# Optimization experiments

Measured on AMD Instinct MI355X. Metric: run time of the kernel, lower is better.

The kernel has to match this reference:

```python
import jax, jax.numpy as jnp
import numpy as np

VOCAB = 32000
WORDVEC = 256
HIDDEN = 512
NULL_TOKEN = 0


def setup_inputs() -> dict:
    key = jax.random.key(0)
    ks = jax.random.split(key, 8)
    N, Tp1 = 16, 257
    captions = jax.random.randint(ks[0], (N, Tp1), 0, VOCAB, dtype=jnp.int64 if jax.config.jax_enable_x64 else jnp.int32)
    W_embed = jax.random.normal(ks[1], (VOCAB, WORDVEC), jnp.float32) / 100.0
    Wx = jax.random.normal(ks[2], (WORDVEC, 4 * HIDDEN), jnp.float32) / np.sqrt(WORDVEC).astype(np.float32)
    Wh = jax.random.normal(ks[3], (HIDDEN, 4 * HIDDEN), jnp.float32) / np.sqrt(HIDDEN).astype(np.float32)
    b = jnp.zeros((4 * HIDDEN,), jnp.float32)
    W_vocab = jax.random.normal(ks[4], (HIDDEN, VOCAB), jnp.float32) / np.sqrt(HIDDEN).astype(np.float32)
    b_vocab = jnp.zeros((VOCAB,), jnp.float32)
    h_init = jax.random.normal(ks[5], (HIDDEN,), jnp.float32)
    return {"captions": captions, "W_embed": W_embed, "Wx": Wx, "Wh": Wh,
            "b": b, "W_vocab": W_vocab, "b_vocab": b_vocab, "h_init": h_init}


def reference(captions, W_embed, Wx, Wh, b, W_vocab, b_vocab, h_init):
    cap_in = captions[:, :-1]   # [N, T]
    cap_out = captions[:, 1:]   # [N, T]
    mask = (cap_out != NULL_TOKEN).astype(jnp.float32)
    N = cap_in.shape[0]
    H = h_init.shape[0]

    # Embedding lookup: [N, T, D]
    x = W_embed[cap_in]
    # Precompute input projections as one big GEMM: [T, N, 4H]
    xw = jnp.einsum('ntd,dk->tnk', x, Wx) + b

    h0 = jnp.tile(h_init, (N, 1))          # [N, H]
    c0 = jnp.zeros_like(h0)                 # lstm_forward starts c at zeros

    def step(carry, a_x):
        h, c = carry
        a = a_x + h @ Wh                    # [N, 4H]
        i, f, o, g = jnp.split(a, 4, axis=-1)
        i = jax.nn.sigmoid(i)
        f = jax.nn.sigmoid(f)
        o = jax.nn.sigmoid(o)
        g = jnp.tanh(g)
        c = f * c + i * g
        h = o * jnp.tanh(c)
        return (h, c), h

    _, hs = jax.lax.scan(step, (h0, c0), xw)  # hs: [T, N, H]

    # Temporal affine: [N, T, V]
    logits = jnp.einsum('tnh,hv->ntv', hs, W_vocab) + b_vocab
    logp = jax.nn.log_softmax(logits, axis=-1)
    nll = -jnp.take_along_axis(logp, cap_out[..., None], axis=-1)[..., 0]
    loss = jnp.sum(nll * mask) / N
    return loss
```

## Files before the change

### kernel.cpp

```cpp
#include <hip/hip_runtime.h>

#define VOCAB   32000
#define WORDVEC 256
#define HIDDEN  512
#define TSTEPS  256
#define NBATCH  16
#define NROWS   (TSTEPS*NBATCH)
#define GATES   (4*HIDDEN)
#define NVB     125
#define NWG     32

typedef __attribute__((ext_vector_type(8))) short short8;
typedef __attribute__((ext_vector_type(4))) float f32x4;
typedef unsigned long long u64;

__device__ __forceinline__ unsigned short f2bf(float x){
    union { float f; unsigned int u; } v; v.f = x;
    unsigned int r = v.u + 0x7fffu + ((v.u >> 16) & 1u);
    return (unsigned short)(r >> 16);
}

__global__ __launch_bounds__(256) void wv_pack(const float* __restrict__ Wv, unsigned short* __restrict__ WvP){
    __shared__ float s[64][65];
    int v0 = blockIdx.x * 64;
    int k0 = blockIdx.y * 64;
    int tid = threadIdx.x;
    for (int i = 0; i < 16; ++i){
        int lin = tid + i*256;
        int kk = lin >> 6, vv = lin & 63;
        s[kk][vv] = Wv[(long)(k0+kk)*VOCAB + v0 + vv];
    }
    __syncthreads();
    for (int i = 0; i < 2; ++i){
        int lr = tid + i*256;
        int f  = lr >> 6;
        int vbl = f >> 1, ktl = f & 1;
        int L = lr & 63, q = L >> 4, ln = L & 15;
        short8 o;
        #pragma unroll
        for (int j = 0; j < 8; ++j)
            o[j] = (short)f2bf(s[ktl*32 + q*8 + j][vbl*16 + ln]);
        long vb = blockIdx.x*4 + vbl;
        long kt = blockIdx.y*2 + ktl;
        *(short8*)(WvP + ((vb*16 + kt)*64 + L)*8) = o;
    }
}

__global__ void whp_prep(const float* __restrict__ Wh, unsigned short* __restrict__ Whp){
    int w = blockIdx.x; int tid = threadIdx.x;
    for (int item = tid; item < 4096; item += 256){
        int f = item >> 6;
        int L = item & 63;
        int kt = f >> 2, nt = f & 3;
        int q = L >> 4, ln = L & 15;
        int col = nt*HIDDEN + w*16 + ln;
        short8 vvec;
        for (int jj = 0; jj < 8; ++jj){
            int k = kt*32 + q*8 + jj;
            vvec[jj] = (short)f2bf(Wh[(long)k*GATES + col]);
        }
        *(short8*)(Whp + ((long)w*4096 + item)*8) = vvec;
    }
}

__global__ void hg_init(const float* __restrict__ h_init, u64* __restrict__ hx){
    int p = blockIdx.x*256 + threadIdx.x;
    int fq = p >> 6;
    int j  = (p & 3) * 2;
    int u0 = (fq>>2)*32 + (fq&3)*8 + j;
    u64 pk = (u64)f2bf(h_init[u0]) | ((u64)f2bf(h_init[u0+1]) << 16);
    hx[p] = pk;
}

__global__ __launch_bounds__(256) void embed_xw(const int* __restrict__ captions,
        const float* __restrict__ Wemb, const float* __restrict__ Wx,
        const float* __restrict__ b, float* __restrict__ xw){
    __shared__ float xs[8][WORDVEC];
    __shared__ int toks[8];
    int tid = threadIdx.x;
    int r0 = blockIdx.x * 8;
    if (tid < 8){
        int r = r0 + tid; int t = r >> 4, n = r & 15;
        toks[tid] = captions[n*257 + t];
    }
    __syncthreads();
    for (int i = 0; i < 8; ++i){
        int lin = tid + i*256;
        int ri = lin >> 8, d = lin & 255;
        xs[ri][d] = Wemb[(long)toks[ri]*WORDVEC + d];
    }
    __syncthreads();
    float4 b0 = *(const float4*)(b + tid*4);
    float4 b1 = *(const float4*)(b + 1024 + tid*4);
    float acc[8][8];
    for (int ri = 0; ri < 8; ++ri){
        acc[ri][0]=b0.x; acc[ri][1]=b0.y; acc[ri][2]=b0.z; acc[ri][3]=b0.w;
        acc[ri][4]=b1.x; acc[ri][5]=b1.y; acc[ri][6]=b1.z; acc[ri][7]=b1.w;
    }
    for (int d = 0; d < WORDVEC; ++d){
        float4 w0 = *(const float4*)(Wx + (long)d*GATES + tid*4);
        float4 w1 = *(const float4*)(Wx + (long)d*GATES + 1024 + tid*4);
        #pragma unroll
        for (int ri = 0; ri < 8; ++ri){
            float xv = xs[ri][d];
            acc[ri][0] += xv*w0.x; acc[ri][1] += xv*w0.y;
            acc[ri][2] += xv*w0.z; acc[ri][3] += xv*w0.w;
            acc[ri][4] += xv*w1.x; acc[ri][5] += xv*w1.y;
            acc[ri][6] += xv*w1.z; acc[ri][7] += xv*w1.w;
        }
    }
    for (int ri = 0; ri < 8; ++ri){
        float4 o0 = {acc[ri][0],acc[ri][1],acc[ri][2],acc[ri][3]};
        float4 o1 = {acc[ri][4],acc[ri][5],acc[ri][6],acc[ri][7]};
        *(float4*)(xw + (long)(r0+ri)*GATES + tid*4) = o0;
        *(float4*)(xw + (long)(r0+ri)*GATES + 1024 + tid*4) = o1;
    }
}

__global__ __launch_bounds__(256) void lstm_mfma(const float* __restrict__ xw,
        const unsigned short* __restrict__ Whp, u64* __restrict__ hx,
        unsigned short* __restrict__ hsP){
    __shared__ unsigned int hstage[4096];
    __shared__ float a_s[4][16][16];
    int w = blockIdx.x;
    int tid = threadIdx.x;
    int wv = tid >> 6;
    int L = tid & 63;
    int q = L >> 4, ln = L & 15;
    int s_idx = tid >> 4, jl = tid & 15;

    short8 bw[16];
    #pragma unroll
    for (int kt = 0; kt < 16; ++kt)
        bw[kt] = *(const short8*)(Whp + ((long)w*4096 + (kt*4+wv)*64 + L)*8);

    float c_r = 0.f;
    int fq_pub = (w>>1)*4 + (w&1)*2 + (jl>>3);
    int pubIdx = fq_pub*64 + s_idx*4 + ((jl>>1)&3);
    int kt_h = w >> 1;
    int q_h  = ((w & 1) << 1) | (jl >> 3);
    int j_h  = jl & 7;

    for (int t = 0; t < TSTEPS; ++t){
        long xb = (long)(t*16 + s_idx)*GATES + w*16 + jl;
        float xg0 = xw[xb], xg1 = xw[xb+512], xg2 = xw[xb+1024], xg3 = xw[xb+1536];

        const u64* hr = hx + (t & 1)*4096;
        u64*       hw = hx + ((t+1) & 1)*4096;

        u64 v[16];
        #pragma unroll
        for (int i = 0; i < 16; ++i)
            v[i] = __hip_atomic_load(hr + tid + i*256, __ATOMIC_RELAXED, __HIP_MEMORY_SCOPE_AGENT);
        for (;;){
            u64 bad = 0;
            #pragma unroll
            for (int i = 0; i < 16; ++i) bad |= (v[i] >> 32) ^ (u64)(unsigned)t;
            if (!bad) break;
            #pragma unroll
            for (int i = 0; i < 16; ++i)
                v[i] = __hip_atomic_load(hr + tid + i*256, __ATOMIC_RELAXED, __HIP_MEMORY_SCOPE_AGENT);
        }
        #pragma unroll
        for (int i = 0; i < 16; ++i) hstage[tid + i*256] = (unsigned)v[i];
        __syncthreads();

        f32x4 acc = {0.f,0.f,0.f,0.f};
        #pragma unroll
        for (int kt = 0; kt < 16; ++kt){
            short8 a = *(const short8*)((const unsigned short*)hstage + (kt*256 + q*64 + ln*4)*2);
            acc = __builtin_amdgcn_mfma_f32_16x16x32_bf16(a, bw[kt], acc, 0, 0, 0);
        }
        #pragma unroll
        for (int r = 0; r < 4; ++r) a_s[wv][q*4 + r][ln] = acc[r];
        __syncthreads();

        float ai = a_s[0][s_idx][jl] + xg0;
        float af = a_s[1][s_idx][jl] + xg1;
        float ao = a_s[2][s_idx][jl] + xg2;
        float ag = a_s[3][s_idx][jl] + xg3;
        float ig = 1.f/(1.f + __expf(-ai));
        float fg = 1.f/(1.f + __expf(-af));
        float og = 1.f/(1.f + __expf(-ao));
        float gg = 2.f/(1.f + __expf(-2.f*ag)) - 1.f;
        c_r = fg*c_r + ig*gg;
        float hv = og * (2.f/(1.f + __expf(-2.f*c_r)) - 1.f);
        unsigned short hb = f2bf(hv);

        int hv32 = (int)hb;
        int other = __shfl(hv32, L ^ 1);
        if ((jl & 1) == 0){
            u64 pk = (u64)(unsigned short)hv32
                   | ((u64)(unsigned short)other << 16)
                   | ((u64)(unsigned)(t+1) << 32);
            __hip_atomic_store(hw + pubIdx, pk, __ATOMIC_RELAXED, __HIP_MEMORY_SCOPE_AGENT);
        }
        int rb = s_idx*16 + (t >> 4);
        hsP[(((long)(rb*16 + kt_h))*64 + q_h*16 + (t & 15))*8 + j_h] = hb;
    }
}

__global__ __launch_bounds__(256) void vocab_gemm(const unsigned short* __restrict__ hsP,
        const unsigned short* __restrict__ WvP, const float* __restrict__ bvoc,
        const int* __restrict__ captions, float* __restrict__ pmax,
        float* __restrict__ psum, float* __restrict__ tlog){
    int bm = blockIdx.x;
    int bn = blockIdx.y;
    int tid = threadIdx.x;
    int wv = tid >> 6, L = tid & 63;
    int q = L >> 4, ln = L & 15;
    __shared__ int   tgt_s[64];
    __shared__ float wmax_s[4][64], wsum_s[4][64];
    if (tid < 64){
        int rg = bm*64 + tid;
        tgt_s[tid] = captions[(rg >> 8)*257 + (rg & 255) + 1];
    }
    __syncthreads();
    f32x4 acc[4][4];
    for (int mt=0;mt<4;++mt) for (int nt=0;nt<4;++nt) acc[mt][nt] = (f32x4){0.f,0.f,0.f,0.f};
    int colb = bn*256 + wv*64;
    const unsigned short* aB = hsP + ((long)(bm*4)*16)*512;
    const unsigned short* bB = WvP + ((long)(bn*16 + wv*4)*16)*512;
    #pragma unroll 4
    for (int kt = 0; kt < 16; ++kt){
        short8 a[4], bb[4];
        #pragma unroll
        for (int mt=0;mt<4;++mt)
            a[mt] = *(const short8*)(aB + ((long)(mt*16 + kt)*64 + L)*8);
        #pragma unroll
        for (int nt=0;nt<4;++nt)
            bb[nt] = *(const short8*)(bB + ((long)(nt*16 + kt)*64 + L)*8);
        #pragma unroll
        for (int mt=0;mt<4;++mt)
            #pragma unroll
            for (int nt=0;nt<4;++nt)
                acc[mt][nt] = __builtin_amdgcn_mfma_f32_16x16x32_bf16(a[mt], bb[nt], acc[mt][nt], 0,0,0);
    }
    float bv[4];
    #pragma unroll
    for (int nt=0;nt<4;++nt) bv[nt] = bvoc[colb + nt*16 + ln];
    #pragma unroll
    for (int mt=0;mt<4;++mt) for (int nt=0;nt<4;++nt) for (int r=0;r<4;++r)
        acc[mt][nt][r] += bv[nt];
    #pragma unroll
    for (int mt=0;mt<4;++mt) for (int r=0;r<4;++r){
        int rl = mt*16 + q*4 + r;
        int tg = tgt_s[rl] - colb;
        if (tg >= 0 && tg < 64){
            int nt = tg >> 4;
            if ((tg & 15) == ln) tlog[bm*64 + rl] = acc[mt][nt][r];
        }
    }
    #pragma unroll
    for (int mt=0;mt<4;++mt){
        #pragma unroll
        for (int r=0;r<4;++r){
            float m = fmaxf(fmaxf(acc[mt][0][r],acc[mt][1][r]), fmaxf(acc[mt][2][r],acc[mt][3][r]));
            for (int d=1; d<16; d<<=1) m = fmaxf(m, __shfl_xor(m, d, 16));
            float s = __expf(acc[mt][0][r]-m) + __expf(acc[mt][1][r]-m)
                    + __expf(acc[mt][2][r]-m) + __expf(acc[mt][3][r]-m);
            for (int d=1; d<16; d<<=1) s += __shfl_xor(s, d, 16);
            if (ln == 0){ int rl = mt*16 + q*4 + r; wmax_s[wv][rl] = m; wsum_s[wv][rl] = s; }
        }
    }
    __syncthreads();
    if (tid < 64){
        float M = fmaxf(fmaxf(wmax_s[0][tid],wmax_s[1][tid]), fmaxf(wmax_s[2][tid],wmax_s[3][tid]));
        float S = 0.f;
        for (int ww=0; ww<4; ++ww) S += wsum_s[ww][tid]*__expf(wmax_s[ww][tid]-M);
        pmax[(long)bn*NROWS + bm*64 + tid] = M;
        psum[(long)bn*NROWS + bm*64 + tid] = S;
    }
}

__global__ __launch_bounds__(256) void reduce_loss(const float* __restrict__ pmax,
        const float* __restrict__ psum, const float* __restrict__ tlog,
        const int* __restrict__ captions, float* __restrict__ out){
    int r = blockIdx.x*256 + threadIdx.x;
    float M = -1e30f;
    for (int p=0;p<NVB;++p) M = fmaxf(M, pmax[(long)p*NROWS + r]);
    float S = 0.f;
    for (int p=0;p<NVB;++p) S += psum[(long)p*NROWS + r]*__expf(pmax[(long)p*NROWS + r]-M);
    float lse = M + logf(S);
    float nll = lse - tlog[r];
    int tok = captions[(r >> 8)*257 + (r & 255) + 1];
    float val = (tok != 0) ? nll : 0.f;
    __shared__ float red[256];
    red[threadIdx.x] = val; __syncthreads();
    for (int s=128; s>0; s>>=1){
        if (threadIdx.x < s) red[threadIdx.x] += red[threadIdx.x+s];
        __syncthreads();
    }
    if (threadIdx.x == 0) atomicAdd(out, red[0] * (1.0f/16.0f));
}

extern "C" void kernel_launch(void* const* d_in, const int* in_sizes, int n_in,
                              void* d_out, int out_size, void* d_ws, size_t ws_size,
                              hipStream_t stream){
    const int*   captions = (const int*)  d_in[0];
    const float* Wemb     = (const float*)d_in[1];
    const float* Wx       = (const float*)d_in[2];
    const float* Wh       = (const float*)d_in[3];
    const float* b        = (const float*)d_in[4];
    const float* Wv       = (const float*)d_in[5];
    const float* bvoc     = (const float*)d_in[6];
    const float* h_init   = (const float*)d_in[7];

    char* ws = (char*)d_ws;
    float*          xw   = (float*)         (ws + 0);
    unsigned short* WvP  = (unsigned short*)(ws + 33554432);
    unsigned short* hsP  = (unsigned short*)(ws + 66322432);
    float*          pmax = (float*)         (ws + 70516736);
    float*          psum = (float*)         (ws + 72564736);
    float*          tlog = (float*)         (ws + 74612736);
    unsigned short* Whp  = (unsigned short*)(ws + 74629120);
    u64*            hx   = (u64*)           (ws + 76726272);

    float* out_f = (float*)d_out;

    (void)hipMemsetAsync(d_out, 0, sizeof(float), stream);

    hipLaunchKernelGGL(wv_pack,      dim3(500, 8), dim3(256), 0, stream, Wv, WvP);
    hipLaunchKernelGGL(whp_prep,     dim3(NWG),    dim3(256), 0, stream, Wh, Whp);
    hipLaunchKernelGGL(hg_init,      dim3(16),     dim3(256), 0, stream, h_init, hx);
    hipLaunchKernelGGL(embed_xw,     dim3(512),    dim3(256), 0, stream, captions, Wemb, Wx, b, xw);
    hipLaunchKernelGGL(lstm_mfma,    dim3(NWG),    dim3(256), 0, stream, xw, Whp, hx, hsP);
    hipLaunchKernelGGL(vocab_gemm,   dim3(64,NVB), dim3(256), 0, stream, hsP, WvP, bvoc, captions, pmax, psum, tlog);
    hipLaunchKernelGGL(reduce_loss,  dim3(16),     dim3(256), 0, stream, pmax, psum, tlog, captions, out_f);
}
```

Measured before the change: 1.147 ms.

## Overlap W_vocab packing with LSTM recurrence, fuse prep kernels, enlarge vocab GEMM tile

The W_vocab bf16 packing blocks now run as extra workgroups in the same launch as the 32 persistent LSTM workgroups, so the serial recurrence, which leaves most CUs idle, overlaps that packing. The embedding/Wx projection, Wh packing and h init kernels are merged into one launch to cut launch gaps. The vocab GEMM tile grows from 64 to 128 rows per block to reuse each W_vocab fragment twice as much, at the cost of higher register pressure. One risk is that the packing blocks may be scheduled ahead of the LSTM blocks, which spin-wait on each other, and this could delay or starve the recurrence.

Measured after the change: 1.534 ms. +33.7%, slower.

```diff
diff --git a/kernel.cpp b/kernel.cpp
--- a/kernel.cpp
+++ b/kernel.cpp
@@ -9,10 +9,13 @@
 #define GATES   (4*HIDDEN)
 #define NVB     125
 #define NWG     32
+#define NWVT    4000
 
 typedef __attribute__((ext_vector_type(8))) short short8;
 typedef __attribute__((ext_vector_type(4))) float f32x4;
 typedef unsigned long long u64;
+
+#define AGLOAD(p) __hip_atomic_load((p), __ATOMIC_RELAXED, __HIP_MEMORY_SCOPE_AGENT)
 
 __device__ __forceinline__ unsigned short f2bf(float x){
     union { float f; unsigned int u; } v; v.f = x;
@@ -20,110 +23,114 @@
     return (unsigned short)(r >> 16);
 }
 
-__global__ __launch_bounds__(256) void wv_pack(const float* __restrict__ Wv, unsigned short* __restrict__ WvP){
-    __shared__ float s[64][65];
-    int v0 = blockIdx.x * 64;
-    int k0 = blockIdx.y * 64;
-    int tid = threadIdx.x;
-    for (int i = 0; i < 16; ++i){
-        int lin = tid + i*256;
-        int kk = lin >> 6, vv = lin & 63;
-        s[kk][vv] = Wv[(long)(k0+kk)*VOCAB + v0 + vv];
-    }
-    __syncthreads();
-    for (int i = 0; i < 2; ++i){
-        int lr = tid + i*256;
-        int f  = lr >> 6;
-        int vbl = f >> 1, ktl = f & 1;
-        int L = lr & 63, q = L >> 4, ln = L & 15;
-        short8 o;
-        #pragma unroll
-        for (int j = 0; j < 8; ++j)
-            o[j] = (short)f2bf(s[ktl*32 + q*8 + j][vbl*16 + ln]);
-        long vb = blockIdx.x*4 + vbl;
-        long kt = blockIdx.y*2 + ktl;
-        *(short8*)(WvP + ((vb*16 + kt)*64 + L)*8) = o;
-    }
-}
-
-__global__ void whp_prep(const float* __restrict__ Wh, unsigned short* __restrict__ Whp){
-    int w = blockIdx.x; int tid = threadIdx.x;
-    for (int item = tid; item < 4096; item += 256){
-        int f = item >> 6;
-        int L = item & 63;
-        int kt = f >> 2, nt = f & 3;
-        int q = L >> 4, ln = L & 15;
-        int col = nt*HIDDEN + w*16 + ln;
-        short8 vvec;
-        for (int jj = 0; jj < 8; ++jj){
-            int k = kt*32 + q*8 + jj;
-            vvec[jj] = (short)f2bf(Wh[(long)k*GATES + col]);
-        }
-        *(short8*)(Whp + ((long)w*4096 + item)*8) = vvec;
-    }
-}
-
-__global__ void hg_init(const float* __restrict__ h_init, u64* __restrict__ hx){
-    int p = blockIdx.x*256 + threadIdx.x;
-    int fq = p >> 6;
-    int j  = (p & 3) * 2;
-    int u0 = (fq>>2)*32 + (fq&3)*8 + j;
-    u64 pk = (u64)f2bf(h_init[u0]) | ((u64)f2bf(h_init[u0+1]) << 16);
-    hx[p] = pk;
-}
-
-__global__ __launch_bounds__(256) void embed_xw(const int* __restrict__ captions,
+__global__ __launch_bounds__(256) void prep_all(const int* __restrict__ captions,
         const float* __restrict__ Wemb, const float* __restrict__ Wx,
-        const float* __restrict__ b, float* __restrict__ xw){
+        const float* __restrict__ b, float* __restrict__ xw,
+        const float* __restrict__ Wh, unsigned short* __restrict__ Whp,
+        const float* __restrict__ h_init, u64* __restrict__ hx){
     __shared__ float xs[8][WORDVEC];
     __shared__ int toks[8];
+    int bid = blockIdx.x;
     int tid = threadIdx.x;
-    int r0 = blockIdx.x * 8;
-    if (tid < 8){
-        int r = r0 + tid; int t = r >> 4, n = r & 15;
-        toks[tid] = captions[n*257 + t];
-    }
-    __syncthreads();
-    for (int i = 0; i < 8; ++i){
-        int lin = tid + i*256;
-        int ri = lin >> 8, d = lin & 255;
-        xs[ri][d] = Wemb[(long)toks[ri]*WORDVEC + d];
-    }
-    __syncthreads();
-    float4 b0 = *(const float4*)(b + tid*4);
-    float4 b1 = *(const float4*)(b + 1024 + tid*4);
-    float acc[8][8];
-    for (int ri = 0; ri < 8; ++ri){
-        acc[ri][0]=b0.x; acc[ri][1]=b0.y; acc[ri][2]=b0.z; acc[ri][3]=b0.w;
-        acc[ri][4]=b1.x; acc[ri][5]=b1.y; acc[ri][6]=b1.z; acc[ri][7]=b1.w;
-    }
-    for (int d = 0; d < WORDVEC; ++d){
-        float4 w0 = *(const float4*)(Wx + (long)d*GATES + tid*4);
-        float4 w1 = *(const float4*)(Wx + (long)d*GATES + 1024 + tid*4);
-        #pragma unroll
+    if (bid < 512){
+        int r0 = bid * 8;
+        if (tid < 8){
+            int r = r0 + tid; int t = r >> 4, n = r & 15;
+            toks[tid] = captions[n*257 + t];
+        }
+        __syncthreads();
+        for (int i = 0; i < 8; ++i){
+            int lin = tid + i*256;
+            int ri = lin >> 8, d = lin & 255;
+            xs[ri][d] = Wemb[(long)toks[ri]*WORDVEC + d];
+        }
+        __syncthreads();
+        float4 b0 = *(const float4*)(b + tid*4);
+        float4 b1 = *(const float4*)(b + 1024 + tid*4);
+        float acc[8][8];
         for (int ri = 0; ri < 8; ++ri){
-            float xv = xs[ri][d];
-            acc[ri][0] += xv*w0.x; acc[ri][1] += xv*w0.y;
-            acc[ri][2] += xv*w0.z; acc[ri][3] += xv*w0.w;
-            acc[ri][4] += xv*w1.x; acc[ri][5] += xv*w1.y;
-            acc[ri][6] += xv*w1.z; acc[ri][7] += xv*w1.w;
-        }
-    }
-    for (int ri = 0; ri < 8; ++ri){
-        float4 o0 = {acc[ri][0],acc[ri][1],acc[ri][2],acc[ri][3]};
-        float4 o1 = {acc[ri][4],acc[ri][5],acc[ri][6],acc[ri][7]};
-        *(float4*)(xw + (long)(r0+ri)*GATES + tid*4) = o0;
-        *(float4*)(xw + (long)(r0+ri)*GATES + 1024 + tid*4) = o1;
-    }
-}
-
-__global__ __launch_bounds__(256) void lstm_mfma(const float* __restrict__ xw,
+            acc[ri][0]=b0.x; acc[ri][1]=b0.y; acc[ri][2]=b0.z; acc[ri][3]=b0.w;
+            acc[ri][4]=b1.x; acc[ri][5]=b1.y; acc[ri][6]=b1.z; acc[ri][7]=b1.w;
+        }
+        for (int d = 0; d < WORDVEC; ++d){
+            float4 w0 = *(const float4*)(Wx + (long)d*GATES + tid*4);
+            float4 w1 = *(const float4*)(Wx + (long)d*GATES + 1024 + tid*4);
+            #pragma unroll
+            for (int ri = 0; ri < 8; ++ri){
+                float xv = xs[ri][d];
+                acc[ri][0] += xv*w0.x; acc[ri][1] += xv*w0.y;
+                acc[ri][2] += xv*w0.z; acc[ri][3] += xv*w0.w;
+                acc[ri][4] += xv*w1.x; acc[ri][5] += xv*w1.y;
+                acc[ri][6] += xv*w1.z; acc[ri][7] += xv*w1.w;
+            }
+        }
+        for (int ri = 0; ri < 8; ++ri){
+            float4 o0 = {acc[ri][0],acc[ri][1],acc[ri][2],acc[ri][3]};
+            float4 o1 = {acc[ri][4],acc[ri][5],acc[ri][6],acc[ri][7]};
+            *(float4*)(xw + (long)(r0+ri)*GATES + tid*4) = o0;
+            *(float4*)(xw + (long)(r0+ri)*GATES + 1024 + tid*4) = o1;
+        }
+    } else if (bid < 544){
+        int w = bid - 512;
+        for (int item = tid; item < 4096; item += 256){
+            int f = item >> 6;
+            int L = item & 63;
+            int kt = f >> 2, nt = f & 3;
+            int q = L >> 4, ln = L & 15;
+            int col = nt*HIDDEN + w*16 + ln;
+            short8 vvec;
+            for (int jj = 0; jj < 8; ++jj){
+                int k = kt*32 + q*8 + jj;
+                vvec[jj] = (short)f2bf(Wh[(long)k*GATES + col]);
+            }
+            *(short8*)(Whp + ((long)w*4096 + item)*8) = vvec;
+        }
+    } else {
+        int p = (bid - 544)*256 + tid;
+        int fq = p >> 6;
+        int j  = (p & 3) * 2;
+        int u0 = (fq>>2)*32 + (fq&3)*8 + j;
+        u64 pk = (u64)f2bf(h_init[u0]) | ((u64)f2bf(h_init[u0+1]) << 16);
+        hx[p] = pk;
+    }
+}
+
+__global__ __launch_bounds__(256) void lstm_wv(const float* __restrict__ xw,
         const unsigned short* __restrict__ Whp, u64* __restrict__ hx,
-        unsigned short* __restrict__ hsP){
+        unsigned short* __restrict__ hsP,
+        const float* __restrict__ Wv, unsigned short* __restrict__ WvP){
     __shared__ unsigned int hstage[4096];
     __shared__ float a_s[4][16][16];
+    __shared__ float s[64][65];
+    int tid = threadIdx.x;
+
+    if (blockIdx.x >= NWG){
+        int tile = blockIdx.x - NWG;
+        int v0 = (tile >> 3) * 64;
+        int k0 = (tile & 7) * 64;
+        for (int i = 0; i < 16; ++i){
+            int lin = tid + i*256;
+            int kk = lin >> 6, vv = lin & 63;
+            s[kk][vv] = Wv[(long)(k0+kk)*VOCAB + v0 + vv];
+        }
+        __syncthreads();
+        for (int i = 0; i < 2; ++i){
+            int lr = tid + i*256;
+            int f  = lr >> 6;
+            int vbl = f >> 1, ktl = f & 1;
+            int L = lr & 63, q = L >> 4, ln = L & 15;
+            short8 o;
+            #pragma unroll
+            for (int j = 0; j < 8; ++j)
+                o[j] = (short)f2bf(s[ktl*32 + q*8 + j][vbl*16 + ln]);
+            long vb = (long)(tile >> 3)*4 + vbl;
+            long kt = (long)(tile & 7)*2 + ktl;
+            *(short8*)(WvP + ((vb*16 + kt)*64 + L)*8) = o;
+        }
+        return;
+    }
+
     int w = blockIdx.x;
-    int tid = threadIdx.x;
     int wv = tid >> 6;
     int L = tid & 63;
     int q = L >> 4, ln = L & 15;
@@ -151,7 +158,7 @@
         u64 v[16];
         #pragma unroll
         for (int i = 0; i < 16; ++i)
-            v[i] = __hip_atomic_load(hr + tid + i*256, __ATOMIC_RELAXED, __HIP_MEMORY_SCOPE_AGENT);
+            v[i] = AGLOAD(hr + tid + i*256);
         for (;;){
             u64 bad = 0;
             #pragma unroll
@@ -159,7 +166,7 @@
             if (!bad) break;
             #pragma unroll
             for (int i = 0; i < 16; ++i)
-                v[i] = __hip_atomic_load(hr + tid + i*256, __ATOMIC_RELAXED, __HIP_MEMORY_SCOPE_AGENT);
+                v[i] = AGLOAD(hr + tid + i*256);
         }
         #pragma unroll
         for (int i = 0; i < 16; ++i) hstage[tid + i*256] = (unsigned)v[i];
@@ -209,29 +216,29 @@
     int tid = threadIdx.x;
     int wv = tid >> 6, L = tid & 63;
     int q = L >> 4, ln = L & 15;
-    __shared__ int   tgt_s[64];
-    __shared__ float wmax_s[4][64], wsum_s[4][64];
-    if (tid < 64){
-        int rg = bm*64 + tid;
+    __shared__ int   tgt_s[128];
+    __shared__ float wmax_s[4][128], wsum_s[4][128];
+    if (tid < 128){
+        int rg = bm*128 + tid;
         tgt_s[tid] = captions[(rg >> 8)*257 + (rg & 255) + 1];
     }
     __syncthreads();
-    f32x4 acc[4][4];
-    for (int mt=0;mt<4;++mt) for (int nt=0;nt<4;++nt) acc[mt][nt] = (f32x4){0.f,0.f,0.f,0.f};
+    f32x4 acc[8][4];
+    for (int mt=0;mt<8;++mt) for (int nt=0;nt<4;++nt) acc[mt][nt] = (f32x4){0.f,0.f,0.f,0.f};
     int colb = bn*256 + wv*64;
-    const unsigned short* aB = hsP + ((long)(bm*4)*16)*512;
+    const unsigned short* aB = hsP + ((long)(bm*8)*16)*512;
     const unsigned short* bB = WvP + ((long)(bn*16 + wv*4)*16)*512;
-    #pragma unroll 4
+    #pragma unroll 2
     for (int kt = 0; kt < 16; ++kt){
-        short8 a[4], bb[4];
-        #pragma unroll
-        for (int mt=0;mt<4;++mt)
+        short8 a[8], bb[4];
+        #pragma unroll
+        for (int mt=0;mt<8;++mt)
             a[mt] = *(const short8*)(aB + ((long)(mt*16 + kt)*64 + L)*8);
         #pragma unroll
         for (int nt=0;nt<4;++nt)
             bb[nt] = *(const short8*)(bB + ((long)(nt*16 + kt)*64 + L)*8);
         #pragma unroll
-        for (int mt=0;mt<4;++mt)
+        for (int mt=0;mt<8;++mt)
             #pragma unroll
             for (int nt=0;nt<4;++nt)
                 acc[mt][nt] = __builtin_amdgcn_mfma_f32_16x16x32_bf16(a[mt], bb[nt], acc[mt][nt], 0,0,0);
@@ -240,19 +247,19 @@
     #pragma unroll
     for (int nt=0;nt<4;++nt) bv[nt] = bvoc[colb + nt*16 + ln];
     #pragma unroll
-    for (int mt=0;mt<4;++mt) for (int nt=0;nt<4;++nt) for (int r=0;r<4;++r)
+    for (int mt=0;mt<8;++mt) for (int nt=0;nt<4;++nt) for (int r=0;r<4;++r)
         acc[mt][nt][r] += bv[nt];
     #pragma unroll
-    for (int mt=0;mt<4;++mt) for (int r=0;r<4;++r){
+    for (int mt=0;mt<8;++mt) for (int r=0;r<4;++r){
         int rl = mt*16 + q*4 + r;
         int tg = tgt_s[rl] - colb;
         if (tg >= 0 && tg < 64){
             int nt = tg >> 4;
-            if ((tg & 15) == ln) tlog[bm*64 + rl] = acc[mt][nt][r];
-        }
-    }
-    #pragma unroll
-    for (int mt=0;mt<4;++mt){
+            if ((tg & 15) == ln) tlog[bm*128 + rl] = acc[mt][nt][r];
+        }
+    }
+    #pragma unroll
+    for (int mt=0;mt<8;++mt){
         #pragma unroll
         for (int r=0;r<4;++r){
             float m = fmaxf(fmaxf(acc[mt][0][r],acc[mt][1][r]), fmaxf(acc[mt][2][r],acc[mt][3][r]));
@@ -264,12 +271,12 @@
         }
     }
     __syncthreads();
-    if (tid < 64){
+    if (tid < 128){
         float M = fmaxf(fmaxf(wmax_s[0][tid],wmax_s[1][tid]), fmaxf(wmax_s[2][tid],wmax_s[3][tid]));
         float S = 0.f;
         for (int ww=0; ww<4; ++ww) S += wsum_s[ww][tid]*__expf(wmax_s[ww][tid]-M);
-        pmax[(long)bn*NROWS + bm*64 + tid] = M;
-        psum[(long)bn*NROWS + bm*64 + tid] = S;
+        pmax[(long)bn*NROWS + bm*128 + tid] = M;
+        psum[(long)bn*NROWS + bm*128 + tid] = S;
     }
 }
 
@@ -320,11 +327,12 @@
 
     (void)hipMemsetAsync(d_out, 0, sizeof(float), stream);
 
-    hipLaunchKernelGGL(wv_pack,      dim3(500, 8), dim3(256), 0, stream, Wv, WvP);
-    hipLaunchKernelGGL(whp_prep,     dim3(NWG),    dim3(256), 0, stream, Wh, Whp);
-    hipLaunchKernelGGL(hg_init,      dim3(16),     dim3(256), 0, stream, h_init, hx);
-    hipLaunchKernelGGL(embed_xw,     dim3(512),    dim3(256), 0, stream, captions, Wemb, Wx, b, xw);
-    hipLaunchKernelGGL(lstm_mfma,    dim3(NWG),    dim3(256), 0, stream, xw, Whp, hx, hsP);
-    hipLaunchKernelGGL(vocab_gemm,   dim3(64,NVB), dim3(256), 0, stream, hsP, WvP, bvoc, captions, pmax, psum, tlog);
-    hipLaunchKernelGGL(reduce_loss,  dim3(16),     dim3(256), 0, stream, pmax, psum, tlog, captions, out_f);
-}
+    hipLaunchKernelGGL(prep_all,     dim3(560),        dim3(256), 0, stream,
+                       captions, Wemb, Wx, b, xw, Wh, Whp, h_init, hx);
+    hipLaunchKernelGGL(lstm_wv,      dim3(NWG+NWVT),   dim3(256), 0, stream,
+                       xw, Whp, hx, hsP, Wv, WvP);
+    hipLaunchKernelGGL(vocab_gemm,   dim3(32,NVB),     dim3(256), 0, stream,
+                       hsP, WvP, bvoc, captions, pmax, psum, tlog);
+    hipLaunchKernelGGL(reduce_loss,  dim3(16),         dim3(256), 0, stream,
+                       pmax, psum, tlog, captions, out_f);
+}
```
